# Kernel tuning notes

Measured on AMD Instinct MI355X. Metric: run time of the kernel, lower is better.

The kernel has to match this reference:

```python
import jax, jax.numpy as jnp
import numpy as np

EMBED_DIM = 2048
NUM_EXPERTS = 64
TOP_K = 2
BATCH = 16384


def setup_inputs() -> dict:
    key = jax.random.key(0)
    kx, kw, kb = jax.random.split(key, 3)
    x = jax.random.normal(kx, (BATCH, EMBED_DIM), dtype=jnp.float32)
    # nn.Linear(embed_dim, num_experts): weight [num_experts, embed_dim], bias [num_experts]
    bound = 1.0 / np.sqrt(EMBED_DIM)
    W = jax.random.uniform(kw, (NUM_EXPERTS, EMBED_DIM), minval=-bound, maxval=bound, dtype=jnp.float32)
    b = jax.random.uniform(kb, (NUM_EXPERTS,), minval=-bound, maxval=bound, dtype=jnp.float32)
    return {"x": x, "W": W, "b": b}


def reference(x, W, b):
    # logits: (batch, num_experts)
    logits = jnp.einsum('bd,ed->be', x, W) + b
    topk_logits, topk_indices = jax.lax.top_k(logits, TOP_K)
    gates = jax.nn.softmax(topk_logits, axis=-1)
    return gates, topk_indices
```

## Files before the change

### kernel.cpp

```cpp
#include <hip/hip_runtime.h>
#include <math.h>

#define EMBED   2048
#define NEXP    64
#define BATCHN  16384
#define RT      32
#define NT_A    256
#define LCAP    16380
#define MARGIN_THRESH 4e-4f

typedef float  f32x4  __attribute__((ext_vector_type(4)));
typedef __bf16 bf16x8 __attribute__((ext_vector_type(8)));

__device__ __forceinline__ void cvt8(const float4& a, const float4& b,
                                     bf16x8& h, bf16x8& l) {
    float f[8] = {a.x, a.y, a.z, a.w, b.x, b.y, b.z, b.w};
    #pragma unroll
    for (int j = 0; j < 8; ++j) {
        __bf16 hh = (__bf16)f[j];
        h[j] = hh;
        l[j] = (__bf16)(f[j] - (float)hh);
    }
}

__global__ __launch_bounds__(256)
void pack_w_kernel(const float* __restrict__ W, __bf16* __restrict__ Wh,
                   __bf16* __restrict__ Wl, int* __restrict__ flagcnt)
{
    const int g = blockIdx.x * 256 + threadIdx.x;
    if (g == 0) *flagcnt = 0;
    const int tile = g >> 12, rem = g & 4095;
    const int kc = rem >> 6, ln = rem & 63;
    const int e = tile * 16 + (ln & 15);
    const int k = kc * 32 + (ln >> 4) * 8;
    const float* wp = W + (size_t)e * EMBED + k;
    float4 a = *(const float4*)wp, b = *(const float4*)(wp + 4);
    bf16x8 h, l;
    cvt8(a, b, h, l);
    *(bf16x8*)(Wh + (size_t)g * 8) = h;
    *(bf16x8*)(Wl + (size_t)g * 8) = l;
}

__global__ __launch_bounds__(NT_A, 2)
void gemm_topk_kernel(const float* __restrict__ x, const __bf16* __restrict__ Wh,
                      const __bf16* __restrict__ Wl, const float* __restrict__ bias,
                      float* __restrict__ out, int* __restrict__ flagcnt,
                      int* __restrict__ flaglist)
{
    __shared__ __align__(16) __bf16 Ah[2][4096];
    __shared__ __align__(16) __bf16 Al[2][4096];
    __shared__ float lg[RT][64];

    const int tid  = threadIdx.x;
    const int lane = tid & 63;
    const int w    = tid >> 6;
    const int row0 = blockIdx.x * RT;

    const float* xr0 = x + (size_t)(row0 + (lane & 15)) * EMBED + w * 32 + (lane >> 4) * 8;
    const float* xr1 = xr0 + (size_t)16 * EMBED;
    const __bf16* whp = Wh + ((size_t)w * 64 * 64 + lane) * 8;
    const __bf16* wlp = Wl + ((size_t)w * 64 * 64 + lane) * 8;

    f32x4 acc0 = {0.f, 0.f, 0.f, 0.f};
    f32x4 acc1 = {0.f, 0.f, 0.f, 0.f};

    {
        bf16x8 h, l;
        cvt8(*(const float4*)xr0, *(const float4*)(xr0 + 4), h, l);
        *(bf16x8*)&Ah[0][tid * 8] = h;
        *(bf16x8*)&Al[0][tid * 8] = l;
        cvt8(*(const float4*)xr1, *(const float4*)(xr1 + 4), h, l);
        *(bf16x8*)&Ah[0][2048 + tid * 8] = h;
        *(bf16x8*)&Al[0][2048 + tid * 8] = l;
    }
    __syncthreads();

    #pragma unroll 1
    for (int s = 0; s < 16; ++s) {
        const int cur = s & 1;
        float4 qa0, qb0, qa1, qb1;
        if (s < 15) {
            qa0 = *(const float4*)(xr0 + (s + 1) * 128);
            qb0 = *(const float4*)(xr0 + (s + 1) * 128 + 4);
            qa1 = *(const float4*)(xr1 + (s + 1) * 128);
            qb1 = *(const float4*)(xr1 + (s + 1) * 128 + 4);
        }
        #pragma unroll
        for (int kc = 0; kc < 4; ++kc) {
            const int ao = (kc * 64 + lane) * 8;
            bf16x8 ah0 = *(bf16x8*)&Ah[cur][ao];
            bf16x8 al0 = *(bf16x8*)&Al[cur][ao];
            bf16x8 ah1 = *(bf16x8*)&Ah[cur][2048 + ao];
            bf16x8 al1 = *(bf16x8*)&Al[cur][2048 + ao];
            bf16x8 bh  = *(const bf16x8*)(whp + (size_t)(s * 4 + kc) * 512);
            bf16x8 bl  = *(const bf16x8*)(wlp + (size_t)(s * 4 + kc) * 512);
            acc0 = __builtin_amdgcn_mfma_f32_16x16x32_bf16(ah0, bh, acc0, 0, 0, 0);
            acc0 = __builtin_amdgcn_mfma_f32_16x16x32_bf16(ah0, bl, acc0, 0, 0, 0);
            acc0 = __builtin_amdgcn_mfma_f32_16x16x32_bf16(al0, bh, acc0, 0, 0, 0);
            acc1 = __builtin_amdgcn_mfma_f32_16x16x32_bf16(ah1, bh, acc1, 0, 0, 0);
            acc1 = __builtin_amdgcn_mfma_f32_16x16x32_bf16(ah1, bl, acc1, 0, 0, 0);
            acc1 = __builtin_amdgcn_mfma_f32_16x16x32_bf16(al1, bh, acc1, 0, 0, 0);
        }
        if (s < 15) {
            bf16x8 h, l;
            cvt8(qa0, qb0, h, l);
            *(bf16x8*)&Ah[cur ^ 1][tid * 8] = h;
            *(bf16x8*)&Al[cur ^ 1][tid * 8] = l;
            cvt8(qa1, qb1, h, l);
            *(bf16x8*)&Ah[cur ^ 1][2048 + tid * 8] = h;
            *(bf16x8*)&Al[cur ^ 1][2048 + tid * 8] = l;
        }
        __syncthreads();
    }

    const float bb = bias[w * 16 + (lane & 15)];
    #pragma unroll
    for (int q = 0; q < 4; ++q) {
        lg[(lane >> 4) * 4 + q][w * 16 + (lane & 15)]      = acc0[q] + bb;
        lg[16 + (lane >> 4) * 4 + q][w * 16 + (lane & 15)] = acc1[q] + bb;
    }
    __syncthreads();

    #pragma unroll 1
    for (int r = 0; r < 8; ++r) {
        const int row_l = w * 8 + r;
        float v1 = lg[row_l][lane], v2 = -INFINITY, v3 = -INFINITY;
        int   i1 = lane, i2 = 0;
        #pragma unroll
        for (int m = 1; m <= 32; m <<= 1) {
            const float o1  = __shfl_xor(v1, m, 64);
            const int   oi1 = __shfl_xor(i1, m, 64);
            const float o2  = __shfl_xor(v2, m, 64);
            const int   oi2 = __shfl_xor(i2, m, 64);
            const float o3  = __shfl_xor(v3, m, 64);
            if (o1 > v1) {
                float nv2; int ni2; float nv3;
                if (v1 > o2) { nv2 = v1; ni2 = i1;  nv3 = fmaxf(v2, o2); }
                else         { nv2 = o2; ni2 = oi2; nv3 = fmaxf(v1, o3); }
                v1 = o1; i1 = oi1; v2 = nv2; i2 = ni2; v3 = nv3;
            } else {
                if (o1 > v2) { v3 = fmaxf(v2, o2); v2 = o1; i2 = oi1; }
                else         { v3 = fmaxf(v3, o1); }
            }
        }
        if (lane == 0) {
            const int row = row0 + row_l;
            const float margin = fminf(v1 - v2, v2 - v3);
            if (margin < MARGIN_THRESH) {
                const int idx = atomicAdd(flagcnt, 1);
                if (idx < LCAP) flaglist[idx] = row;
            }
            const float e2  = __expf(v2 - v1);
            const float inv = 1.0f / (1.0f + e2);
            *(float2*)&out[row * 2]              = make_float2(inv, e2 * inv);
            *(float2*)&out[2 * BATCHN + row * 2] = make_float2((float)i1, (float)i2);
        }
    }
}

__global__ __launch_bounds__(256, 2)
void recheck_kernel(const float* __restrict__ x, const float* __restrict__ W,
                    const float* __restrict__ bias, float* __restrict__ out,
                    const int* __restrict__ flagcnt, const int* __restrict__ flaglist)
{
    __shared__ double sh[NEXP];
    const int tid = threadIdx.x;
    const int e = tid >> 2, q = tid & 3;
    int cnt = *flagcnt;
    if (cnt > LCAP) cnt = LCAP;

    #pragma unroll 1
    for (int i = blockIdx.x; i < cnt; i += gridDim.x) {
        const int row = flaglist[i];
        const float* xr = x + (size_t)row * EMBED + q * 512;
        const float* wr = W + (size_t)e * EMBED + q * 512;
        double s = 0.0;
        #pragma unroll 4
        for (int k = 0; k < 512; k += 4) {
            const float4 xv = *(const float4*)(xr + k);
            const float4 wv = *(const float4*)(wr + k);
            s += (double)xv.x * (double)wv.x;
            s += (double)xv.y * (double)wv.y;
            s += (double)xv.z * (double)wv.z;
            s += (double)xv.w * (double)wv.w;
        }
        s += __shfl_xor(s, 1, 64);
        s += __shfl_xor(s, 2, 64);
        if (q == 0) sh[e] = s + (double)bias[e];
        __syncthreads();
        if (tid == 0) {
            double v1 = -1e300, v2 = -1e300; int i1 = 0, i2 = 0;
            for (int ee = 0; ee < NEXP; ++ee) {
                const double v = sh[ee];
                if (v > v1)      { v2 = v1; i2 = i1; v1 = v; i1 = ee; }
                else if (v > v2) { v2 = v; i2 = ee; }
            }
            const double ex  = exp(v2 - v1);
            const double inv = 1.0 / (1.0 + ex);
            out[row * 2]                  = (float)inv;
            out[row * 2 + 1]              = (float)(ex * inv);
            out[2 * BATCHN + row * 2]     = (float)i1;
            out[2 * BATCHN + row * 2 + 1] = (float)i2;
        }
        __syncthreads();
    }
}

extern "C" void kernel_launch(void* const* d_in, const int* in_sizes, int n_in,
                              void* d_out, int out_size, void* d_ws, size_t ws_size,
                              hipStream_t stream) {
    const float* x = (const float*)d_in[0];
    const float* W = (const float*)d_in[1];
    const float* b = (const float*)d_in[2];
    float* out = (float*)d_out;
    int*    flagcnt  = (int*)d_ws;
    int*    flaglist = flagcnt + 4;
    __bf16* Wh = (__bf16*)((char*)d_ws + 65536);
    __bf16* Wl = (__bf16*)((char*)d_ws + 65536 + 262144);
    pack_w_kernel   <<<dim3(64),          dim3(256),  0, stream>>>(W, Wh, Wl, flagcnt);
    gemm_topk_kernel<<<dim3(BATCHN / RT), dim3(NT_A), 0, stream>>>(x, Wh, Wl, b, out, flagcnt, flaglist);
    recheck_kernel  <<<dim3(128),         dim3(256),  0, stream>>>(x, W, b, out, flagcnt, flaglist);
}
```

Before: 240.4 us.

## Stream x tiles directly into LDS via global_load_lds and convert at use

Replaces the register-staged prefetch of x (global load, bf16 hi/lo split, LDS store) with direct global-to-LDS async loads of raw fp32 into an XOR-swizzled double buffer. The bf16 split now runs per k-chunk right before the MFMAs, reading swizzled float4s from LDS. This is meant to drop the register round trip and VGPR pressure of the prefetch and to hide load latency behind the MFMAs. In exchange, LDS holds fp32 instead of bf16, so reads are twice as wide. The conversion work moves into the inner loop, and correctness depends on the swizzle and the global_load_lds wait semantics across the barrier.

```diff
diff --git a/kernel.cpp b/kernel.cpp
--- a/kernel.cpp
+++ b/kernel.cpp
@@ -21,6 +21,13 @@
         h[j] = hh;
         l[j] = (__bf16)(f[j] - (float)hh);
     }
+}
+
+__device__ __forceinline__ void gload_lds16(const float* g, float* lds) {
+    __builtin_amdgcn_global_load_lds(
+        (const __attribute__((address_space(1))) unsigned int*)g,
+        (__attribute__((address_space(3))) unsigned int*)lds,
+        16, 0, 0);
 }
 
 __global__ __launch_bounds__(256)
@@ -47,8 +54,7 @@
                       float* __restrict__ out, int* __restrict__ flagcnt,
                       int* __restrict__ flaglist)
 {
-    __shared__ __align__(16) __bf16 Ah[2][4096];
-    __shared__ __align__(16) __bf16 Al[2][4096];
+    __shared__ __align__(16) float Xs[2][RT * 128];
     __shared__ float lg[RT][64];
 
     const int tid  = threadIdx.x;
@@ -56,59 +62,57 @@
     const int w    = tid >> 6;
     const int row0 = blockIdx.x * RT;
 
-    const float* xr0 = x + (size_t)(row0 + (lane & 15)) * EMBED + w * 32 + (lane >> 4) * 8;
-    const float* xr1 = xr0 + (size_t)16 * EMBED;
+    const float* gsrc[4];
+    #pragma unroll
+    for (int i = 0; i < 4; ++i) {
+        const int d   = (w * 4 + i) * 64 + lane;
+        const int row = d >> 5;
+        const int cu  = (d & 31) ^ (row & 7);
+        gsrc[i] = x + (size_t)(row0 + row) * EMBED + cu * 4;
+    }
+
     const __bf16* whp = Wh + ((size_t)w * 64 * 64 + lane) * 8;
     const __bf16* wlp = Wl + ((size_t)w * 64 * 64 + lane) * 8;
 
     f32x4 acc0 = {0.f, 0.f, 0.f, 0.f};
     f32x4 acc1 = {0.f, 0.f, 0.f, 0.f};
 
-    {
-        bf16x8 h, l;
-        cvt8(*(const float4*)xr0, *(const float4*)(xr0 + 4), h, l);
-        *(bf16x8*)&Ah[0][tid * 8] = h;
-        *(bf16x8*)&Al[0][tid * 8] = l;
-        cvt8(*(const float4*)xr1, *(const float4*)(xr1 + 4), h, l);
-        *(bf16x8*)&Ah[0][2048 + tid * 8] = h;
-        *(bf16x8*)&Al[0][2048 + tid * 8] = l;
-    }
+    #pragma unroll
+    for (int i = 0; i < 4; ++i)
+        gload_lds16(gsrc[i], &Xs[0][(w * 4 + i) * 256]);
     __syncthreads();
+
+    const int r0i = lane & 15;
+    const int r1i = r0i + 16;
+    const int sw  = r0i & 7;
 
     #pragma unroll 1
     for (int s = 0; s < 16; ++s) {
         const int cur = s & 1;
-        float4 qa0, qb0, qa1, qb1;
         if (s < 15) {
-            qa0 = *(const float4*)(xr0 + (s + 1) * 128);
-            qb0 = *(const float4*)(xr0 + (s + 1) * 128 + 4);
-            qa1 = *(const float4*)(xr1 + (s + 1) * 128);
-            qb1 = *(const float4*)(xr1 + (s + 1) * 128 + 4);
-        }
+            #pragma unroll
+            for (int i = 0; i < 4; ++i)
+                gload_lds16(gsrc[i] + (s + 1) * 128, &Xs[cur ^ 1][(w * 4 + i) * 256]);
+        }
+        const float* xs = &Xs[cur][0];
         #pragma unroll
         for (int kc = 0; kc < 4; ++kc) {
-            const int ao = (kc * 64 + lane) * 8;
-            bf16x8 ah0 = *(bf16x8*)&Ah[cur][ao];
-            bf16x8 al0 = *(bf16x8*)&Al[cur][ao];
-            bf16x8 ah1 = *(bf16x8*)&Ah[cur][2048 + ao];
-            bf16x8 al1 = *(bf16x8*)&Al[cur][2048 + ao];
-            bf16x8 bh  = *(const bf16x8*)(whp + (size_t)(s * 4 + kc) * 512);
-            bf16x8 bl  = *(const bf16x8*)(wlp + (size_t)(s * 4 + kc) * 512);
+            const int cb = kc * 8 + ((lane >> 4) & 3) * 2;
+            float4 a0 = *(const float4*)&xs[r0i * 128 + ((cb    ) ^ sw) * 4];
+            float4 b0 = *(const float4*)&xs[r0i * 128 + ((cb + 1) ^ sw) * 4];
+            float4 a1 = *(const float4*)&xs[r1i * 128 + ((cb    ) ^ sw) * 4];
+            float4 b1 = *(const float4*)&xs[r1i * 128 + ((cb + 1) ^ sw) * 4];
+            bf16x8 ah0, al0, ah1, al1;
+            cvt8(a0, b0, ah0, al0);
+            cvt8(a1, b1, ah1, al1);
+            bf16x8 bh = *(const bf16x8*)(whp + (size_t)(s * 4 + kc) * 512);
+            bf16x8 bl = *(const bf16x8*)(wlp + (size_t)(s * 4 + kc) * 512);
             acc0 = __builtin_amdgcn_mfma_f32_16x16x32_bf16(ah0, bh, acc0, 0, 0, 0);
             acc0 = __builtin_amdgcn_mfma_f32_16x16x32_bf16(ah0, bl, acc0, 0, 0, 0);
             acc0 = __builtin_amdgcn_mfma_f32_16x16x32_bf16(al0, bh, acc0, 0, 0, 0);
             acc1 = __builtin_amdgcn_mfma_f32_16x16x32_bf16(ah1, bh, acc1, 0, 0, 0);
             acc1 = __builtin_amdgcn_mfma_f32_16x16x32_bf16(ah1, bl, acc1, 0, 0, 0);
             acc1 = __builtin_amdgcn_mfma_f32_16x16x32_bf16(al1, bh, acc1, 0, 0, 0);
-        }
-        if (s < 15) {
-            bf16x8 h, l;
-            cvt8(qa0, qb0, h, l);
-            *(bf16x8*)&Ah[cur ^ 1][tid * 8] = h;
-            *(bf16x8*)&Al[cur ^ 1][tid * 8] = l;
-            cvt8(qa1, qb1, h, l);
-            *(bf16x8*)&Ah[cur ^ 1][2048 + tid * 8] = h;
-            *(bf16x8*)&Al[cur ^ 1][2048 + tid * 8] = l;
         }
         __syncthreads();
     }
```

Result: no change. 240.8 us (+0.1%).
